# Kernel tuning notes

Hardware: AMD Instinct MI355X
Metric: run time of the kernel (lower is better)

Reference implementation:

```python
import jax, jax.numpy as jnp
import numpy as np

B, QL, CTX, H = 1, 2048, 2048, 4096
NH, NKV, HD = 32, 8, 128


def rotate_half(x):
    x1, x2 = jnp.split(x, 2, axis=-1)
    return jnp.concatenate([-x2, x1], axis=-1)


def apply_rotary(x, cos, sin):
    # x: [B, h, S, HD]; cos/sin: [B, S, HD] -> broadcast over heads
    cos = cos[:, None, :, :]
    sin = sin[:, None, :, :]
    return x * cos + rotate_half(x) * sin


def setup_inputs() -> dict:
    key = jax.random.key(0)
    ks = jax.random.split(key, 8)
    s = 0.02
    return {
        "hidden_states": jax.random.normal(ks[0], (B, QL, H), jnp.float32),
        "target_hidden": jax.random.normal(ks[1], (B, CTX, H), jnp.float32),
        "cos": jax.random.uniform(ks[2], (B, CTX + QL, HD), jnp.float32),
        "sin": jax.random.uniform(ks[3], (B, CTX + QL, HD), jnp.float32),
        "Wq": jax.random.normal(ks[4], (NH * HD, H), jnp.float32) * s,
        "Wk": jax.random.normal(ks[5], (NKV * HD, H), jnp.float32) * s,
        "Wv": jax.random.normal(ks[6], (NKV * HD, H), jnp.float32) * s,
        "Wo": jax.random.normal(ks[7], (H, NH * HD), jnp.float32) * s,
    }


def reference(hidden_states, target_hidden, cos, sin, Wq, Wk, Wv, Wo):
    bsz, q_len, _ = hidden_states.shape
    ctx_len = target_hidden.shape[1]

    def proj(x, W, nh):  # [B,S,H] @ W.T -> [B,nh,S,HD]
        y = jnp.einsum("bsh,dh->bsd", x, W)
        return y.reshape(bsz, x.shape[1], nh, HD).transpose(0, 2, 1, 3)

    q = proj(hidden_states, Wq, NH)
    k_ctx = proj(target_hidden, Wk, NKV)
    v_ctx = proj(target_hidden, Wv, NKV)
    k_noise = proj(hidden_states, Wk, NKV)
    v_noise = proj(hidden_states, Wv, NKV)

    cos_n = cos[:, ctx_len:ctx_len + q_len]
    sin_n = sin[:, ctx_len:ctx_len + q_len]
    q = apply_rotary(q, cos_n, sin_n)
    k_noise = apply_rotary(k_noise, cos_n, sin_n)
    k_ctx = apply_rotary(k_ctx, cos[:, :ctx_len], sin[:, :ctx_len])

    k = jnp.concatenate([k_ctx, k_noise], axis=2)  # [B,NKV,CTX+QL,HD]
    v = jnp.concatenate([v_ctx, v_noise], axis=2)

    n_rep = NH // NKV
    k = jnp.repeat(k, n_rep, axis=1)  # repeat_interleave on head dim
    v = jnp.repeat(v, n_rep, axis=1)

    scale = 1.0 / jnp.sqrt(jnp.asarray(HD, q.dtype))
    scores = jnp.einsum("bhqd,bhkd->bhqk", q, k) * scale
    probs = jax.nn.softmax(scores, axis=-1)
    attn = jnp.einsum("bhqk,bhkd->bhqd", probs, v)
    attn = attn.transpose(0, 2, 1, 3).reshape(bsz, q_len, NH * HD)
    return jnp.einsum("bsd,hd->bsh", attn, Wo)
```

## Files before the change

### kernel.cpp

```cpp
#include <hip/hip_runtime.h>

typedef unsigned short u16;
typedef _Float16 f16;
typedef _Float16 f16x4 __attribute__((ext_vector_type(4)));
typedef _Float16 f16x8 __attribute__((ext_vector_type(8)));
typedef float f32x4 __attribute__((ext_vector_type(4)));

#define GLL16(gptr, lptr)                                                        \
  __builtin_amdgcn_global_load_lds(                                              \
      (const __attribute__((address_space(1))) void*)(gptr),                     \
      (__attribute__((address_space(3))) void*)(lptr), 16, 0, 0)

__global__ void cast_all_k(const float* __restrict__ h, const float* __restrict__ t,
                           const float* __restrict__ wq, const float* __restrict__ wk,
                           const float* __restrict__ wv, const float* __restrict__ wo,
                           f16* __restrict__ Xcat, f16* __restrict__ Wqb,
                           f16* __restrict__ Wkvb, f16* __restrict__ Wob) {
  long i = (long)blockIdx.x * 256 + threadIdx.x;
  const float* s; f16* d; long off;
  if (i < 2097152)        { s = h;  d = Xcat;            off = i; }
  else if (i < 4194304)   { s = t;  d = Xcat + 8388608;  off = i - 2097152; }
  else if (i < 8388608)   { s = wq; d = Wqb;             off = i - 4194304; }
  else if (i < 9437184)   { s = wk; d = Wkvb;            off = i - 8388608; }
  else if (i < 10485760)  { s = wv; d = Wkvb + 4194304;  off = i - 9437184; }
  else                    { s = wo; d = Wob;             off = i - 10485760; }
  float4 v = *(const float4*)(s + off * 4);
  f16x4 o;
  o.x = (f16)v.x; o.y = (f16)v.y; o.z = (f16)v.z; o.w = (f16)v.w;
  *(f16x4*)(d + off * 4) = o;
}

template <int MODE>
__global__ __launch_bounds__(512, 2) void gemm8k(
    const f16* __restrict__ Xcat, const f16* __restrict__ Wqb,
    const f16* __restrict__ Wkvb, const float* __restrict__ cosT,
    const float* __restrict__ sinT, f16* __restrict__ Qb, f16* __restrict__ Kb,
    f16* __restrict__ Vt, const f16* __restrict__ Ao,
    const f16* __restrict__ Wob, float* __restrict__ Cp, float qscale) {
  __shared__ __align__(16) f16 lds[65536];
  const int tid = threadIdx.x;
  const int w = tid >> 6, lane = tid & 63;
  const int quad = lane >> 4, l16 = lane & 15;
  const int wm = w >> 1, wn = w & 1;

  int b = (int)blockIdx.x;
  int l = ((b & 7) << 5) | (b >> 3);

  const f16 *A, *B;
  long tM, tN;
  int NT, kbeg;
  bool isQ = false, isV = false;
  float* Cz = nullptr;
  if (MODE == 0) {
    kbeg = 0; NT = 64;
    if (l < 128) {
      A = Xcat; B = Wqb; tM = (long)(l >> 4) * 256; tN = (long)(l & 15) * 256;
      isQ = true;
    } else {
      int l2 = l - 128;
      A = Xcat; B = Wkvb; tM = (long)(l2 >> 3) * 256; tN = (long)(l2 & 7) * 256;
      isV = (tN >= 1024);
    }
  } else {
    int z = l >> 7, r0 = l & 127;
    A = Ao; B = Wob; tM = (long)(r0 >> 4) * 256; tN = (long)(r0 & 15) * 256;
    kbeg = z * 2048; NT = 32; Cz = Cp + (long)z * 8388608;
  }

  const int sr8 = lane >> 3;
  const int cg = (lane & 7) ^ sr8;
  const f16* Ag = A + (tM + 16 * w + sr8) * 4096 + kbeg + cg * 8;
  const f16* Bg = B + (tN + 16 * w + sr8) * 4096 + kbeg + cg * 8;
  const int ldsw = w * 1024;

#define STAGE_A(hf, t, c)                                                      \
  do {                                                                         \
    const f16* g_ = Ag + (long)(t) * 64 + (long)(hf) * (128 * 4096);           \
    f16* d_ = &lds[(c) * 16384 + (hf) * 8192 + ldsw];                          \
    GLL16(g_, d_);                                                             \
    GLL16(g_ + 8 * 4096, d_ + 512);                                            \
  } while (0)
#define STAGE_B(hf, t, c)                                                      \
  do {                                                                         \
    const f16* g_ = Bg + (long)(t) * 64 + (long)(hf) * (128 * 4096);           \
    f16* d_ = &lds[32768 + (c) * 16384 + (hf) * 8192 + ldsw];                  \
    GLL16(g_, d_);                                                             \
    GLL16(g_ + 8 * 4096, d_ + 512);                                            \
  } while (0)

  const int rA = wm * 64 + l16;
  const int rB = wn * 128 + l16;
  const int sw = l16 & 7;
#define LDA(fr, mi, kk, c)                                                     \
  fr = *(const f16x8*)&lds[(c) * 16384 + (rA + (mi) * 16) * 64 +               \
                           (((kk) * 4 + quad) ^ sw) * 8]
#define LDB(fr, ni, kk, c)                                                     \
  fr = *(const f16x8*)&lds[32768 + (c) * 16384 + (rB + (ni) * 16) * 64 +       \
                           (((kk) * 4 + quad) ^ sw) * 8]

#define MFMA16 __builtin_amdgcn_mfma_f32_16x16x32_f16
#define BAR() __builtin_amdgcn_s_barrier()
#define WAITDS()                                                               \
  do {                                                                         \
    asm volatile("s_waitcnt lgkmcnt(0)" ::: "memory");                         \
    __builtin_amdgcn_sched_barrier(0);                                         \
  } while (0)

  f32x4 acc[4][8] = {};
  f16x8 af[2][2], bf0[4][2], bf1[4][2];

  STAGE_B(0, 0, 0); STAGE_B(1, 0, 0); STAGE_A(0, 0, 0); STAGE_A(1, 0, 0);
  STAGE_B(0, 1, 1); STAGE_B(1, 1, 1);
  asm volatile("s_waitcnt vmcnt(4)" ::: "memory");
  BAR();

#define TILE_STEP(t, c)                                                        \
  do {                                                                         \
                                       \
    LDA(af[0][0], 0, 0, c); LDA(af[0][1], 0, 1, c);                            \
    LDA(af[1][0], 1, 0, c); LDA(af[1][1], 1, 1, c);                            \
    LDB(bf0[0][0], 0, 0, c); LDB(bf0[0][1], 0, 1, c);                          \
    LDB(bf0[1][0], 1, 0, c); LDB(bf0[1][1], 1, 1, c);                          \
    LDB(bf0[2][0], 2, 0, c); LDB(bf0[2][1], 2, 1, c);                          \
    LDB(bf0[3][0], 3, 0, c); LDB(bf0[3][1], 3, 1, c);                          \
    if ((t) + 1 < NT) STAGE_A(0, (t) + 1, (c) ^ 1);                            \
    BAR(); WAITDS();                                                           \
    __builtin_amdgcn_s_setprio(1);                                             \
    _Pragma("unroll") for (int mi = 0; mi < 2; ++mi)                           \
        _Pragma("unroll") for (int ni = 0; ni < 4; ++ni) {                     \
      acc[mi][ni] = MFMA16(af[mi][0], bf0[ni][0], acc[mi][ni], 0, 0, 0);       \
      acc[mi][ni] = MFMA16(af[mi][1], bf0[ni][1], acc[mi][ni], 0, 0, 0);       \
    }                                                                          \
    __builtin_amdgcn_s_setprio(0);                                             \
    BAR();                                                                     \
                                       \
    LDB(bf1[0][0], 4, 0, c); LDB(bf1[0][1], 4, 1, c);                          \
    LDB(bf1[1][0], 5, 0, c); LDB(bf1[1][1], 5, 1, c);                          \
    LDB(bf1[2][0], 6, 0, c); LDB(bf1[2][1], 6, 1, c);                          \
    LDB(bf1[3][0], 7, 0, c); LDB(bf1[3][1], 7, 1, c);                          \
    if ((t) + 1 < NT) STAGE_A(1, (t) + 1, (c) ^ 1);                            \
    BAR(); WAITDS();                                                           \
    __builtin_amdgcn_s_setprio(1);                                             \
    _Pragma("unroll") for (int mi = 0; mi < 2; ++mi)                           \
        _Pragma("unroll") for (int ni = 0; ni < 4; ++ni) {                     \
      acc[mi][4 + ni] =                                                        \
          MFMA16(af[mi][0], bf1[ni][0], acc[mi][4 + ni], 0, 0, 0);             \
      acc[mi][4 + ni] =                                                        \
          MFMA16(af[mi][1], bf1[ni][1], acc[mi][4 + ni], 0, 0, 0);             \
    }                                                                          \
    __builtin_amdgcn_s_setprio(0);                                             \
    BAR();                                                                     \
            \
    LDA(af[0][0], 2, 0, c); LDA(af[0][1], 2, 1, c);                            \
    LDA(af[1][0], 3, 0, c); LDA(af[1][1], 3, 1, c);                            \
    if ((t) + 2 < NT) STAGE_B(0, (t) + 2, c);                                  \
    BAR(); WAITDS();                                                           \
    __builtin_amdgcn_s_setprio(1);                                             \
    _Pragma("unroll") for (int mi = 0; mi < 2; ++mi)                           \
        _Pragma("unroll") for (int ni = 0; ni < 4; ++ni) {                     \
      acc[2 + mi][ni] = MFMA16(af[mi][0], bf0[ni][0], acc[2 + mi][ni], 0, 0, 0);\
      acc[2 + mi][ni] = MFMA16(af[mi][1], bf0[ni][1], acc[2 + mi][ni], 0, 0, 0);\
    }                                                                          \
    __builtin_amdgcn_s_setprio(0);                                             \
    BAR();                                                                     \
      \
    if ((t) + 2 < NT) STAGE_B(1, (t) + 2, c);                                  \
    BAR();                                                                     \
    __builtin_amdgcn_s_setprio(1);                                             \
    _Pragma("unroll") for (int mi = 0; mi < 2; ++mi)                           \
        _Pragma("unroll") for (int ni = 0; ni < 4; ++ni) {                     \
      acc[2 + mi][4 + ni] =                                                    \
          MFMA16(af[mi][0], bf1[ni][0], acc[2 + mi][4 + ni], 0, 0, 0);         \
      acc[2 + mi][4 + ni] =                                                    \
          MFMA16(af[mi][1], bf1[ni][1], acc[2 + mi][4 + ni], 0, 0, 0);         \
    }                                                                          \
    __builtin_amdgcn_s_setprio(0);                                             \
    if ((t) + 2 < NT)                                                          \
      asm volatile("s_waitcnt vmcnt(4)" ::: "memory");                         \
    else                                                                       \
      asm volatile("s_waitcnt vmcnt(0)" ::: "memory");                         \
    BAR();                                                                     \
  } while (0)

  for (int t = 0; t < NT; t += 2) {
    TILE_STEP(t, 0);
    TILE_STEP(t + 1, 1);
  }

  if (MODE == 1) {
#pragma unroll
    for (int mi = 0; mi < 4; ++mi)
#pragma unroll
      for (int ni = 0; ni < 8; ++ni)
#pragma unroll
        for (int r = 0; r < 4; ++r) {
          long row = tM + wm * 64 + mi * 16 + quad * 4 + r;
          long col = tN + wn * 128 + ni * 16 + l16;
          Cz[row * 4096 + col] = acc[mi][ni][r];
        }
  } else if (isV) {
    const int kvh = (int)((tN - 1024) >> 7) + wn;
#pragma unroll
    for (int mi = 0; mi < 4; ++mi) {
      int key0 = ((int)tM + wm * 64 + mi * 16 + quad * 4) ^ 2048;
#pragma unroll
      for (int ni = 0; ni < 8; ++ni) {
        int d = ni * 16 + l16;
        f16x4 pk;
#pragma unroll
        for (int r = 0; r < 4; ++r) pk[r] = (f16)acc[mi][ni][r];
        *(f16x4*)&Vt[((long)kvh * 128 + d) * 4096 + key0] = pk;
      }
    }
  } else {
    const float sc = isQ ? qscale : 1.0f;
    const int h = (int)(tN >> 7) + wn;
#pragma unroll
    for (int mi = 0; mi < 4; ++mi)
#pragma unroll
      for (int r = 0; r < 4; ++r) {
        int rg = (int)tM + wm * 64 + mi * 16 + quad * 4 + r;
        int pos = isQ ? (2048 + rg) : (rg ^ 2048);
        const float* cp = cosT + (long)pos * 128;
        const float* sp = sinT + (long)pos * 128;
        f16* orow = isQ ? Qb + ((long)h * 2048 + rg) * 128
                        : Kb + ((long)h * 4096 + pos) * 128;
#pragma unroll
        for (int ni = 0; ni < 4; ++ni) {
          int d = ni * 16 + l16;
          float x0 = acc[mi][ni][r], x1 = acc[mi][ni + 4][r];
          orow[d] = (f16)((x0 * cp[d] - x1 * sp[d]) * sc);
          orow[d + 64] = (f16)((x1 * cp[d + 64] + x0 * sp[d + 64]) * sc);
        }
      }
  }
#undef TILE_STEP
#undef STAGE_A
#undef STAGE_B
#undef LDA
#undef LDB
#undef WAITDS
#undef BAR
#undef MFMA16
}

__global__ __launch_bounds__(256, 2) void flash_k(const f16* __restrict__ Qb,
                                                  const f16* __restrict__ Kb,
                                                  const f16* __restrict__ Vt,
                                                  f16* __restrict__ Ob) {
  __shared__ __align__(16) f16 Ks[64 * 128];
  __shared__ __align__(16) f16 Vs[128 * 64];
  __shared__ __align__(16) f16 Ps[4][32 * 72];
  const int tid = threadIdx.x;
  const int w = tid >> 6, lane = tid & 63;
  const int quad = lane >> 4, l16 = lane & 15;
  const int h = blockIdx.y;
  const int kvh = h >> 2;
  const int q0 = blockIdx.x * 128;

  f16x8 qf[2][4];
#pragma unroll
  for (int mi = 0; mi < 2; ++mi) {
    const f16* qrow = Qb + ((long)h * 2048 + q0 + w * 32 + mi * 16 + l16) * 128 + quad * 8;
#pragma unroll
    for (int kc = 0; kc < 4; ++kc) qf[mi][kc] = *(const f16x8*)(qrow + kc * 32);
  }

  f32x4 of[2][8] = {};
  float lsum[2] = {0.f, 0.f};
  const f16* Kg = Kb + (long)kvh * 4096 * 128;
  const f16* Vg = Vt + (long)kvh * 128 * 4096;
  f16* PsW = &Ps[w][0];

  const int krow_in_wave = (lane >> 4);
  const int kslot = lane & 15;
  const int vrow_in_wave = (lane >> 3);
  const int vslot = lane & 7;
  const int vgc = vslot ^ (vrow_in_wave & 7);

  for (int kt = 0; kt < 64; ++kt) {
    __syncthreads();
#pragma unroll
    for (int it = 0; it < 4; ++it) {
      int row = w * 16 + it * 4 + krow_in_wave;
      int gc = kslot ^ (it * 4 + krow_in_wave);
      GLL16(Kg + (long)(kt * 64 + row) * 128 + gc * 8, &Ks[(w * 16 + it * 4) * 128]);
    }
#pragma unroll
    for (int it = 0; it < 4; ++it) {
      int row = w * 32 + it * 8 + vrow_in_wave;
      GLL16(Vg + (long)row * 4096 + kt * 64 + vgc * 8, &Vs[(w * 32 + it * 8) * 64]);
    }
    __syncthreads();
    f32x4 s[2][4] = {};
#pragma unroll
    for (int nt = 0; nt < 4; ++nt) {
      f16x8 ak[4];
#pragma unroll
      for (int kc = 0; kc < 4; ++kc) {
        int slot = (kc * 4 + quad) ^ l16;
        ak[kc] = *(const f16x8*)&Ks[(nt * 16 + l16) * 128 + slot * 8];
      }
#pragma unroll
      for (int mi = 0; mi < 2; ++mi)
#pragma unroll
        for (int kc = 0; kc < 4; ++kc)
          s[mi][nt] = __builtin_amdgcn_mfma_f32_16x16x32_f16(ak[kc], qf[mi][kc],
                                                             s[mi][nt], 0, 0, 0);
    }
#pragma unroll
    for (int mi = 0; mi < 2; ++mi)
#pragma unroll
      for (int nt = 0; nt < 4; ++nt) {
        f16x4 pk;
#pragma unroll
        for (int r = 0; r < 4; ++r) {
          float pv = __builtin_amdgcn_exp2f(s[mi][nt][r]);
          lsum[mi] += pv;
          pk[r] = (f16)pv;
        }
        *(f16x4*)&PsW[(mi * 16 + l16) * 72 + nt * 16 + quad * 4] = pk;
      }
#pragma unroll
    for (int kc2 = 0; kc2 < 2; ++kc2) {
      f16x8 bp[2];
#pragma unroll
      for (int mi = 0; mi < 2; ++mi)
        bp[mi] = *(const f16x8*)&PsW[(mi * 16 + l16) * 72 + kc2 * 32 + quad * 8];
#pragma unroll
      for (int dt = 0; dt < 8; ++dt) {
        int slot = (kc2 * 4 + quad) ^ (l16 & 7);
        f16x8 av = *(const f16x8*)&Vs[(dt * 16 + l16) * 64 + slot * 8];
#pragma unroll
        for (int mi = 0; mi < 2; ++mi)
          of[mi][dt] =
              __builtin_amdgcn_mfma_f32_16x16x32_f16(av, bp[mi], of[mi][dt], 0, 0, 0);
      }
    }
  }
#pragma unroll
  for (int mi = 0; mi < 2; ++mi) {
    float v = lsum[mi];
    v += __shfl_xor(v, 16, 64);
    v += __shfl_xor(v, 32, 64);
    float inv = 1.0f / v;
    long q = q0 + w * 32 + mi * 16 + l16;
#pragma unroll
    for (int dt = 0; dt < 8; ++dt) {
      f16x4 o4;
#pragma unroll
      for (int r = 0; r < 4; ++r) o4[r] = (f16)(of[mi][dt][r] * inv);
      *(f16x4*)&Ob[q * 4096 + h * 128 + dt * 16 + quad * 4] = o4;
    }
  }
}

__global__ void reduce2_k(const float* __restrict__ p, float* __restrict__ out) {
  long i = ((long)blockIdx.x * 256 + threadIdx.x) * 4;
  float4 a = *(const float4*)(p + i);
  float4 b = *(const float4*)(p + 8388608 + i);
  a.x += b.x; a.y += b.y; a.z += b.z; a.w += b.w;
  *(float4*)(out + i) = a;
}

extern "C" void kernel_launch(void* const* d_in, const int* in_sizes, int n_in,
                              void* d_out, int out_size, void* d_ws, size_t ws_size,
                              hipStream_t stream) {
  (void)in_sizes; (void)n_in; (void)out_size; (void)ws_size;
  const float* hidden = (const float*)d_in[0];
  const float* target = (const float*)d_in[1];
  const float* cosT = (const float*)d_in[2];
  const float* sinT = (const float*)d_in[3];
  const float* Wq = (const float*)d_in[4];
  const float* Wk = (const float*)d_in[5];
  const float* Wv = (const float*)d_in[6];
  const float* Wo = (const float*)d_in[7];
  float* out = (float*)d_out;

  char* p = (char*)d_ws;
  auto alloc = [&](size_t bytes) {
    char* r = p;
    p += (bytes + 255) & ~(size_t)255;
    return r;
  };
  f16* Xcat = (f16*)alloc(4096ull * 4096 * 2);
  f16* Wqb  = (f16*)alloc(4096ull * 4096 * 2);
  f16* Wkvb = (f16*)alloc(2048ull * 4096 * 2);
  f16* Wob  = (f16*)alloc(4096ull * 4096 * 2);
  f16* Qb   = (f16*)alloc(32ull * 2048 * 128 * 2);
  f16* Kb   = (f16*)alloc(8ull * 4096 * 128 * 2);
  f16* Vt   = (f16*)alloc(8ull * 128 * 4096 * 2);
  f16* Ao   = (f16*)alloc(2048ull * 4096 * 2);
  float* Pp = (float*)d_ws;

  cast_all_k<<<57344, 256, 0, stream>>>(hidden, target, Wq, Wk, Wv, Wo,
                                        Xcat, Wqb, Wkvb, Wob);

  const float QSC = (float)(0.08838834764831845 * 1.4426950408889634);
  gemm8k<0><<<256, 512, 0, stream>>>(Xcat, Wqb, Wkvb, cosT, sinT, Qb, Kb, Vt,
                                     nullptr, nullptr, nullptr, QSC);

  flash_k<<<dim3(16, 32), 256, 0, stream>>>(Qb, Kb, Vt, Ao);

  gemm8k<1><<<256, 512, 0, stream>>>(nullptr, nullptr, nullptr, nullptr, nullptr,
                                     nullptr, nullptr, nullptr, Ao, Wob, Pp, 0.f);
  reduce2_k<<<8192, 256, 0, stream>>>(Pp, out);
}
```

Before: 592.5 us.

## Double-buffer K tiles and overlap loads with compute in flash attention

The flash kernel now double-buffers the K tile in LDS and prefetches the next K tile while computing softmax. The V tile load is issued at the start of the iteration and waited on only before the PV matmul, using explicit vmcnt waits and raw barriers. MFMA sections run at raised wave priority. The grid is remapped to 1-D so that consecutive blocks cover different KV heads, which is meant to spread K/V reuse across the GPU's L2 caches. This raises LDS use (an extra 16KB for K), which could reduce occupancy. The hand-tuned vmcnt counts must match the number of outstanding loads exactly, or the results are wrong.

```diff
diff --git a/kernel.cpp b/kernel.cpp
--- a/kernel.cpp
+++ b/kernel.cpp
@@ -150,7 +150,7 @@
     }                                                                          \
     __builtin_amdgcn_s_setprio(0);                                             \
     BAR();                                                                     \
-            \
+                                       \
     LDA(af[0][0], 2, 0, c); LDA(af[0][1], 2, 1, c);                            \
     LDA(af[1][0], 3, 0, c); LDA(af[1][1], 3, 1, c);                            \
     if ((t) + 2 < NT) STAGE_B(0, (t) + 2, c);                                  \
@@ -248,15 +248,17 @@
                                                   const f16* __restrict__ Kb,
                                                   const f16* __restrict__ Vt,
                                                   f16* __restrict__ Ob) {
-  __shared__ __align__(16) f16 Ks[64 * 128];
+  __shared__ __align__(16) f16 Ks[2][64 * 128];
   __shared__ __align__(16) f16 Vs[128 * 64];
   __shared__ __align__(16) f16 Ps[4][32 * 72];
   const int tid = threadIdx.x;
   const int w = tid >> 6, lane = tid & 63;
   const int quad = lane >> 4, l16 = lane & 15;
-  const int h = blockIdx.y;
-  const int kvh = h >> 2;
-  const int q0 = blockIdx.x * 128;
+  const int b = blockIdx.x;
+  const int kvh = b & 7;
+  const int j = b >> 3;
+  const int h = kvh * 4 + (j >> 4);
+  const int q0 = (j & 15) * 128;
 
   f16x8 qf[2][4];
 #pragma unroll
@@ -272,34 +274,50 @@
   const f16* Vg = Vt + (long)kvh * 128 * 4096;
   f16* PsW = &Ps[w][0];
 
-  const int krow_in_wave = (lane >> 4);
+  const int krow = (lane >> 4);
   const int kslot = lane & 15;
-  const int vrow_in_wave = (lane >> 3);
+  const int vrow = (lane >> 3);
   const int vslot = lane & 7;
-  const int vgc = vslot ^ (vrow_in_wave & 7);
+  const int vgc = vslot ^ (vrow & 7);
+
+#define FBAR() __builtin_amdgcn_s_barrier()
+#define STAGE_K(kt_, c_)                                                       \
+  do {                                                                         \
+    _Pragma("unroll") for (int it = 0; it < 4; ++it) {                         \
+      int row = w * 16 + it * 4 + krow;                                        \
+      int gc = kslot ^ (it * 4 + krow);                                        \
+      GLL16(Kg + (long)((kt_)*64 + row) * 128 + gc * 8,                        \
+            &Ks[c_][(w * 16 + it * 4) * 128]);                                 \
+    }                                                                          \
+  } while (0)
+#define STAGE_V(kt_)                                                           \
+  do {                                                                         \
+    _Pragma("unroll") for (int it = 0; it < 4; ++it) {                         \
+      int row = w * 32 + it * 8 + vrow;                                        \
+      GLL16(Vg + (long)row * 4096 + (kt_)*64 + vgc * 8,                        \
+            &Vs[(w * 32 + it * 8) * 64]);                                      \
+    }                                                                          \
+  } while (0)
+
+  STAGE_K(0, 0);
 
   for (int kt = 0; kt < 64; ++kt) {
-    __syncthreads();
-#pragma unroll
-    for (int it = 0; it < 4; ++it) {
-      int row = w * 16 + it * 4 + krow_in_wave;
-      int gc = kslot ^ (it * 4 + krow_in_wave);
-      GLL16(Kg + (long)(kt * 64 + row) * 128 + gc * 8, &Ks[(w * 16 + it * 4) * 128]);
-    }
-#pragma unroll
-    for (int it = 0; it < 4; ++it) {
-      int row = w * 32 + it * 8 + vrow_in_wave;
-      GLL16(Vg + (long)row * 4096 + kt * 64 + vgc * 8, &Vs[(w * 32 + it * 8) * 64]);
-    }
-    __syncthreads();
+    const int c = kt & 1;
+    FBAR();
+    STAGE_V(kt);
+    asm volatile("s_waitcnt vmcnt(4)" ::: "memory");
+    FBAR();
+    __builtin_amdgcn_sched_barrier(0);
+
     f32x4 s[2][4] = {};
+    __builtin_amdgcn_s_setprio(1);
 #pragma unroll
     for (int nt = 0; nt < 4; ++nt) {
       f16x8 ak[4];
 #pragma unroll
       for (int kc = 0; kc < 4; ++kc) {
         int slot = (kc * 4 + quad) ^ l16;
-        ak[kc] = *(const f16x8*)&Ks[(nt * 16 + l16) * 128 + slot * 8];
+        ak[kc] = *(const f16x8*)&Ks[c][(nt * 16 + l16) * 128 + slot * 8];
       }
 #pragma unroll
       for (int mi = 0; mi < 2; ++mi)
@@ -308,6 +326,10 @@
           s[mi][nt] = __builtin_amdgcn_mfma_f32_16x16x32_f16(ak[kc], qf[mi][kc],
                                                              s[mi][nt], 0, 0, 0);
     }
+    __builtin_amdgcn_s_setprio(0);
+
+    if (kt < 63) STAGE_K(kt + 1, c ^ 1);
+
 #pragma unroll
     for (int mi = 0; mi < 2; ++mi)
 #pragma unroll
@@ -321,6 +343,15 @@
         }
         *(f16x4*)&PsW[(mi * 16 + l16) * 72 + nt * 16 + quad * 4] = pk;
       }
+
+    if (kt < 63)
+      asm volatile("s_waitcnt vmcnt(4)" ::: "memory");
+    else
+      asm volatile("s_waitcnt vmcnt(0)" ::: "memory");
+    FBAR();
+    __builtin_amdgcn_sched_barrier(0);
+
+    __builtin_amdgcn_s_setprio(1);
 #pragma unroll
     for (int kc2 = 0; kc2 < 2; ++kc2) {
       f16x8 bp[2];
@@ -337,7 +368,12 @@
               __builtin_amdgcn_mfma_f32_16x16x32_f16(av, bp[mi], of[mi][dt], 0, 0, 0);
       }
     }
-  }
+    __builtin_amdgcn_s_setprio(0);
+  }
+#undef STAGE_K
+#undef STAGE_V
+#undef FBAR
+
 #pragma unroll
   for (int mi = 0; mi < 2; ++mi) {
     float v = lsum[mi];
@@ -400,7 +436,7 @@
   gemm8k<0><<<256, 512, 0, stream>>>(Xcat, Wqb, Wkvb, cosT, sinT, Qb, Kb, Vt,
                                      nullptr, nullptr, nullptr, QSC);
 
-  flash_k<<<dim3(16, 32), 256, 0, stream>>>(Qb, Kb, Vt, Ao);
+  flash_k<<<512, 256, 0, stream>>>(Qb, Kb, Vt, Ao);
 
   gemm8k<1><<<256, 512, 0, stream>>>(nullptr, nullptr, nullptr, nullptr, nullptr,
                                      nullptr, nullptr, nullptr, Ao, Wob, Pp, 0.f);
```

Measured after the change: 582.7 us. No clear change (-1.7%).
